# Performance work log

Measured on AMD Instinct MI355X. Metric: run time of the kernel, lower is better.

Reference implementation:

```python
import jax, jax.numpy as jnp
import numpy as np

N = 4096   # n_roi
E = 131072 # edges (avg degree 32)
B = 64     # batch of subjects/windows sharing one connectome
K = 4      # Chebyshev order


def _cheb_params(key, cin, cout):
    kw, kb = jax.random.split(key)
    w = jax.random.normal(kw, (K, cin, cout), dtype=jnp.float32) / np.sqrt(K * cin)
    b = jax.random.normal(kb, (cout,), dtype=jnp.float32) * 0.01
    return w, b


def _lin_params(key, cin, cout):
    kw, kb = jax.random.split(key)
    w = jax.random.normal(kw, (cin, cout), dtype=jnp.float32) / np.sqrt(cin)
    b = jax.random.normal(kb, (cout,), dtype=jnp.float32) * 0.01
    return w, b


def setup_inputs() -> dict:
    key = jax.random.key(0)
    ks = jax.random.split(key, 12)
    x = jax.random.normal(ks[0], (B, N, 1), dtype=jnp.float32)
    src = jax.random.randint(ks[1], (E,), 0, N, dtype=jnp.int32)
    dst = jax.random.randint(ks[2], (E,), 0, N, dtype=jnp.int32)
    edge_weight = jax.random.uniform(ks[3], (E,), dtype=jnp.float32)
    w1, b1 = _cheb_params(ks[4], 1, 32)
    w2, b2 = _cheb_params(ks[5], 32, 32)
    w3, b3 = _cheb_params(ks[6], 32, 32)
    w4, b4 = _cheb_params(ks[7], 32, 32)
    w5, b5 = _cheb_params(ks[8], 32, 4)
    fw1, fb1 = _lin_params(ks[9], N * 4, 128)
    fw2, fb2 = _lin_params(ks[10], 128, 128)
    fw3, fb3 = _lin_params(ks[11], 128, 9)
    return dict(x=x, src=src, dst=dst, edge_weight=edge_weight,
                w1=w1, b1=b1, w2=w2, b2=b2, w3=w3, b3=b3,
                w4=w4, b4=b4, w5=w5, b5=b5,
                fw1=fw1, fb1=fb1, fw2=fw2, fb2=fb2, fw3=fw3, fb3=fb3)


def _norm_weights(src, dst, edge_weight):
    # PyG ChebConv default: sym normalization, lambda_max=2 ->
    # L_hat = -D^{-1/2} A D^{-1/2}, diagonal 2/lambda_max - 1 = 0 (self-loop skipped)
    deg = jax.ops.segment_sum(edge_weight, src, num_segments=N)
    dinv = jnp.where(deg > 0, jax.lax.rsqrt(jnp.maximum(deg, 1e-30)), 0.0)
    return -dinv[src] * edge_weight * dinv[dst]


def _propagate(z, src, dst, nw):
    # z: [B, N, C] -> L_hat @ z  via gather-multiply-scatter over edges
    msg = nw[None, :, None] * z[:, src, :]          # [B, E, C]
    msg = jnp.swapaxes(msg, 0, 1)                    # [E, B, C]
    agg = jax.ops.segment_sum(msg, dst, num_segments=N)  # [N, B, C]
    return jnp.swapaxes(agg, 0, 1)                   # [B, N, C]


def _cheb_conv(x, src, dst, nw, w, b):
    # x: [B,N,Cin], w: [K,Cin,Cout]
    tx0 = x
    out = jnp.einsum('bni,io->bno', tx0, w[0])
    tx1 = _propagate(tx0, src, dst, nw)
    out = out + jnp.einsum('bni,io->bno', tx1, w[1])
    for k in range(2, K):
        tx2 = 2.0 * _propagate(tx1, src, dst, nw) - tx0
        out = out + jnp.einsum('bni,io->bno', tx2, w[k])
        tx0, tx1 = tx1, tx2
    return out + b


def reference(x, src, dst, edge_weight, w1, b1, w2, b2, w3, b3, w4, b4, w5, b5,
              fw1, fb1, fw2, fb2, fw3, fb3):
    nw = _norm_weights(src, dst, edge_weight)
    h = jax.nn.relu(_cheb_conv(x, src, dst, nw, w1, b1))
    h = jax.nn.relu(_cheb_conv(h, src, dst, nw, w2, b2))
    h = jax.nn.relu(_cheb_conv(h, src, dst, nw, w3, b3))
    h = jax.nn.relu(_cheb_conv(h, src, dst, nw, w4, b4))
    h = jax.nn.relu(_cheb_conv(h, src, dst, nw, w5, b5))  # [B, N, 4]
    h = h.reshape(B, N * 4)
    # original has dropout (identity at eval) and NO relu between fc layers
    h = h @ fw1 + fb1
    h = h @ fw2 + fb2
    return h @ fw3 + fb3  # [B, 9]
```

## Files before the change

### kernel.cpp

```cpp
#include <hip/hip_runtime.h>
#include <cstdint>

#define NN 4096
#define EE 131072
#define BB 64
#define EPAD (EE + 8 * NN)

typedef float f4 __attribute__((ext_vector_type(4)));
typedef short bf16x8 __attribute__((ext_vector_type(8)));
typedef unsigned int u4 __attribute__((ext_vector_type(4)));
typedef unsigned int u2 __attribute__((ext_vector_type(2)));
typedef unsigned short ushort_t;
typedef unsigned int uint_t;

__device__ __forceinline__ void up8(u4 u, f4& lo, f4& hi) {
    lo.x = __uint_as_float(u.x << 16);
    lo.y = __uint_as_float(u.x & 0xffff0000u);
    lo.z = __uint_as_float(u.y << 16);
    lo.w = __uint_as_float(u.y & 0xffff0000u);
    hi.x = __uint_as_float(u.z << 16);
    hi.y = __uint_as_float(u.z & 0xffff0000u);
    hi.z = __uint_as_float(u.w << 16);
    hi.w = __uint_as_float(u.w & 0xffff0000u);
}
__device__ __forceinline__ uint_t bfpk(float a, float b) {
    uint_t xa = __float_as_uint(a); xa = (xa + 0x7fffu + ((xa >> 16) & 1u)) >> 16;
    uint_t xb = __float_as_uint(b); xb = (xb + 0x7fffu + ((xb >> 16) & 1u));
    return (xa & 0xffffu) | (xb & 0xffff0000u);
}


__global__ void k_deg_hist(const int* __restrict__ src, const int* __restrict__ dst,
                           const float* __restrict__ ew, float* __restrict__ deg,
                           int* __restrict__ cnt) {
    int e = blockIdx.x * blockDim.x + threadIdx.x;
    if (e >= EE) return;
    atomicAdd(&deg[src[e]], ew[e]);
    atomicAdd(&cnt[dst[e]], 1);
}

__global__ __launch_bounds__(1024) void k_scan(const int* __restrict__ cnt,
                                               int* __restrict__ rowptr,
                                               int* __restrict__ cursor) {
    __shared__ int s[1024];
    int tid = threadIdx.x;
    int p0 = (cnt[tid * 4 + 0] + 7) & ~7;
    int p1 = (cnt[tid * 4 + 1] + 7) & ~7;
    int p2 = (cnt[tid * 4 + 2] + 7) & ~7;
    int p3 = (cnt[tid * 4 + 3] + 7) & ~7;
    int sum = p0 + p1 + p2 + p3;
    s[tid] = sum;
    __syncthreads();
    for (int off = 1; off < 1024; off <<= 1) {
        int t = (tid >= off) ? s[tid - off] : 0;
        __syncthreads();
        s[tid] += t;
        __syncthreads();
    }
    int excl = s[tid] - sum;
    rowptr[tid * 4 + 0] = excl; cursor[tid * 4 + 0] = excl; excl += p0;
    rowptr[tid * 4 + 1] = excl; cursor[tid * 4 + 1] = excl; excl += p1;
    rowptr[tid * 4 + 2] = excl; cursor[tid * 4 + 2] = excl; excl += p2;
    rowptr[tid * 4 + 3] = excl; cursor[tid * 4 + 3] = excl; excl += p3;
    if (tid == 1023) rowptr[4096] = excl;
}

__global__ void k_fill(const int* __restrict__ src, const int* __restrict__ dst,
                       const float* __restrict__ ew, const float* __restrict__ deg,
                       int* __restrict__ cursor, int2* __restrict__ cv) {
    int e = blockIdx.x * blockDim.x + threadIdx.x;
    if (e >= EE) return;
    int s = src[e], d = dst[e];
    int pos = atomicAdd(&cursor[d], 1);
    float ds = deg[s], dd = deg[d];
    float is = ds > 0.f ? rsqrtf(fmaxf(ds, 1e-30f)) : 0.f;
    float id = dd > 0.f ? rsqrtf(fmaxf(dd, 1e-30f)) : 0.f;
    float v = -(is * ew[e] * id);
    cv[pos] = make_int2(s, __float_as_int(v));
}

__global__ __launch_bounds__(256) void k_packw(const float* __restrict__ w2,
                                               const float* __restrict__ w3,
                                               const float* __restrict__ w4,
                                               const float* __restrict__ w5,
                                               uint_t* __restrict__ Wb) {
    int idx = blockIdx.x * 256 + threadIdx.x;
    int L = idx >> 11, rem = idx & 2047;
    int kk = rem >> 9, r2 = rem & 511, co = r2 >> 4, u = r2 & 15;
    float lo, hi;
    if (L < 3) {
        const float* W = (L == 0) ? w2 : (L == 1) ? w3 : w4;
        lo = W[kk * 1024 + (2 * u) * 32 + co];
        hi = W[kk * 1024 + (2 * u + 1) * 32 + co];
    } else {
        lo = (co < 4) ? w5[kk * 128 + (2 * u) * 4 + co] : 0.f;
        hi = (co < 4) ? w5[kk * 128 + (2 * u + 1) * 4 + co] : 0.f;
    }
    Wb[idx] = bfpk(lo, hi);
}

__global__ __launch_bounds__(256) void k_transpose_x(const float* __restrict__ x,
                                                     float* __restrict__ X0) {
    __shared__ float s[64 * 65];
    int n0 = blockIdx.x * 64;
    for (int idx = threadIdx.x; idx < 4096; idx += 256) {
        int b = idx >> 6, nl = idx & 63;
        s[nl * 65 + b] = x[(size_t)b * NN + n0 + nl];
    }
    __syncthreads();
    for (int idx = threadIdx.x; idx < 4096; idx += 256) {
        int nl = idx >> 6, b = idx & 63;
        X0[(size_t)(n0 + nl) * 64 + b] = s[nl * 65 + b];
    }
}

__global__ __launch_bounds__(64) void k_spmm_narrow(const int* __restrict__ rowptr,
                                                    const int2* __restrict__ cv,
                                                    const float* __restrict__ Zin,
                                                    const float* __restrict__ Tprev,
                                                    float* __restrict__ Tout,
                                                    float alpha, int useprev) {
    int n = blockIdx.x;
    int lane = threadIdx.x;
    int start = rowptr[n], end = rowptr[n + 1];
    float acc = 0.f;
    for (int e = start; e < end; e += 8) {
        const int4* q = reinterpret_cast<const int4*>(cv + e);
        int4 a = q[0], b = q[1], c = q[2], d = q[3];
        float z0 = Zin[((size_t)a.x << 6) + lane];
        float z1 = Zin[((size_t)a.z << 6) + lane];
        float z2 = Zin[((size_t)b.x << 6) + lane];
        float z3 = Zin[((size_t)b.z << 6) + lane];
        float z4 = Zin[((size_t)c.x << 6) + lane];
        float z5 = Zin[((size_t)c.z << 6) + lane];
        float z6 = Zin[((size_t)d.x << 6) + lane];
        float z7 = Zin[((size_t)d.z << 6) + lane];
        acc += __int_as_float(a.y) * z0 + __int_as_float(a.w) * z1
             + __int_as_float(b.y) * z2 + __int_as_float(b.w) * z3
             + __int_as_float(c.y) * z4 + __int_as_float(c.w) * z5
             + __int_as_float(d.y) * z6 + __int_as_float(d.w) * z7;
    }
    size_t o = ((size_t)n << 6) + lane;
    float r = alpha * acc;
    if (useprev) r -= Tprev[o];
    Tout[o] = r;
}

__global__ __launch_bounds__(256) void k_expand1(const float* __restrict__ T0,
                                                 const float* __restrict__ T1,
                                                 const float* __restrict__ T2,
                                                 const float* __restrict__ T3,
                                                 const float* __restrict__ w1,
                                                 const float* __restrict__ b1,
                                                 ushort_t* __restrict__ H) {
    __shared__ float sT[4][64];
    __shared__ float sW[128];
    __shared__ float sB[32];
    int n = blockIdx.x, tid = threadIdx.x;
    {
        int k = tid >> 6, b = tid & 63;
        const float* Tk = (k == 0) ? T0 : (k == 1) ? T1 : (k == 2) ? T2 : T3;
        sT[k][b] = Tk[(size_t)n * 64 + b];
    }
    if (tid < 128) sW[tid] = w1[tid];
    if (tid < 32) sB[tid] = b1[tid];
    __syncthreads();
    int chunk = tid >> 6, blk = tid & 63;
    int b_g = chunk * 16 + (blk & 15);
    int co0 = (blk >> 4) * 8;
    float t0 = sT[0][b_g], t1 = sT[1][b_g], t2 = sT[2][b_g], t3 = sT[3][b_g];
    float r[8];
#pragma unroll
    for (int j = 0; j < 8; ++j) {
        int co = co0 + j;
        float v = t0 * sW[co] + t1 * sW[32 + co] + t2 * sW[64 + co] + t3 * sW[96 + co] + sB[co];
        r[j] = v > 0.f ? v : 0.f;
    }
    u4 st;
    st.x = bfpk(r[0], r[1]); st.y = bfpk(r[2], r[3]);
    st.z = bfpk(r[4], r[5]); st.w = bfpk(r[6], r[7]);
    *reinterpret_cast<u4*>(H + (size_t)n * 2048 + tid * 8) = st;
}

__global__ __launch_bounds__(256, 4) void k_spmm_pure(const int* __restrict__ rowptr,
                                                      const int2* __restrict__ cv,
                                                      const ushort_t* __restrict__ Zg,
                                                      const ushort_t* __restrict__ Pown,
                                                      ushort_t* __restrict__ Tout) {
    int chunk = blockIdx.x & 3;
    int rowblk = blockIdx.x >> 2;
    int wave = threadIdx.x >> 6;
    int lane = threadIdx.x & 63;
    int n = rowblk * 4 + wave;
    int col0 = chunk * 512 + lane * 8;

    int start = rowptr[n], end = rowptr[n + 1];
    f4 aL0 = {0,0,0,0}, aH0 = {0,0,0,0}, aL1 = {0,0,0,0}, aH1 = {0,0,0,0};
    for (int e = start; e < end; e += 8) {
        const int4* q = reinterpret_cast<const int4*>(cv + e);
        int4 a = q[0], b = q[1], c = q[2], d = q[3];
        u4 u0 = *reinterpret_cast<const u4*>(Zg + (((size_t)a.x) << 11) + col0);
        u4 u1 = *reinterpret_cast<const u4*>(Zg + (((size_t)a.z) << 11) + col0);
        u4 u2 = *reinterpret_cast<const u4*>(Zg + (((size_t)b.x) << 11) + col0);
        u4 u3 = *reinterpret_cast<const u4*>(Zg + (((size_t)b.z) << 11) + col0);
        u4 u4_ = *reinterpret_cast<const u4*>(Zg + (((size_t)c.x) << 11) + col0);
        u4 u5 = *reinterpret_cast<const u4*>(Zg + (((size_t)c.z) << 11) + col0);
        u4 u6 = *reinterpret_cast<const u4*>(Zg + (((size_t)d.x) << 11) + col0);
        u4 u7 = *reinterpret_cast<const u4*>(Zg + (((size_t)d.z) << 11) + col0);
        f4 lo, hi;
        up8(u0, lo, hi);  aL0 += __int_as_float(a.y) * lo; aH0 += __int_as_float(a.y) * hi;
        up8(u1, lo, hi);  aL1 += __int_as_float(a.w) * lo; aH1 += __int_as_float(a.w) * hi;
        up8(u2, lo, hi);  aL0 += __int_as_float(b.y) * lo; aH0 += __int_as_float(b.y) * hi;
        up8(u3, lo, hi);  aL1 += __int_as_float(b.w) * lo; aH1 += __int_as_float(b.w) * hi;
        up8(u4_, lo, hi); aL0 += __int_as_float(c.y) * lo; aH0 += __int_as_float(c.y) * hi;
        up8(u5, lo, hi);  aL1 += __int_as_float(c.w) * lo; aH1 += __int_as_float(c.w) * hi;
        up8(u6, lo, hi);  aL0 += __int_as_float(d.y) * lo; aH0 += __int_as_float(d.y) * hi;
        up8(u7, lo, hi);  aL1 += __int_as_float(d.w) * lo; aH1 += __int_as_float(d.w) * hi;
    }
    size_t o = (((size_t)n) << 11) + col0;
    f4 tL = aL0 + aL1, tH = aH0 + aH1;
    if (Pown) {
        u4 pu = *reinterpret_cast<const u4*>(Pown + o);
        f4 pL, pH;
        up8(pu, pL, pH);
        tL = 2.f * tL - pL;
        tH = 2.f * tH - pH;
    }
    u4 st;
    st.x = bfpk(tL.x, tL.y); st.y = bfpk(tL.z, tL.w);
    st.z = bfpk(tH.x, tH.y); st.w = bfpk(tH.z, tH.w);
    *reinterpret_cast<u4*>(Tout + o) = st;
}

template <int COUT>
__global__ __launch_bounds__(256, 4) void k_cheb_mfma(
    const int* __restrict__ rowptr, const int2* __restrict__ cv,
    const ushort_t* __restrict__ T2g,
    const ushort_t* __restrict__ T1,
    const ushort_t* __restrict__ H,
    const uint_t* __restrict__ Wb,
    const float* __restrict__ bias,
    void* __restrict__ OUTv)
{
    int chunk = blockIdx.x & 3;
    int rowblk = blockIdx.x >> 2;
    int wave = threadIdx.x >> 6;
    int lane = threadIdx.x & 63;
    int n = rowblk * 4 + wave;
    int b16 = lane & 15, qk = lane >> 4;
    int col0 = chunk * 512 + lane * 8;
    size_t o = (((size_t)n) << 11) + col0;

    u4 a1 = *reinterpret_cast<const u4*>(T1 + o);
    u4 a2 = *reinterpret_cast<const u4*>(T2g + o);
    u4 a0 = *reinterpret_cast<const u4*>(H + o);

    int start = rowptr[n], end = rowptr[n + 1];
    f4 aL0 = {0,0,0,0}, aH0 = {0,0,0,0}, aL1 = {0,0,0,0}, aH1 = {0,0,0,0};
    for (int e = start; e < end; e += 8) {
        const int4* q = reinterpret_cast<const int4*>(cv + e);
        int4 a = q[0], b = q[1], c = q[2], d = q[3];
        u4 u0 = *reinterpret_cast<const u4*>(T2g + (((size_t)a.x) << 11) + col0);
        u4 u1 = *reinterpret_cast<const u4*>(T2g + (((size_t)a.z) << 11) + col0);
        u4 u2 = *reinterpret_cast<const u4*>(T2g + (((size_t)b.x) << 11) + col0);
        u4 u3 = *reinterpret_cast<const u4*>(T2g + (((size_t)b.z) << 11) + col0);
        u4 u4_ = *reinterpret_cast<const u4*>(T2g + (((size_t)c.x) << 11) + col0);
        u4 u5 = *reinterpret_cast<const u4*>(T2g + (((size_t)c.z) << 11) + col0);
        u4 u6 = *reinterpret_cast<const u4*>(T2g + (((size_t)d.x) << 11) + col0);
        u4 u7 = *reinterpret_cast<const u4*>(T2g + (((size_t)d.z) << 11) + col0);
        f4 lo, hi;
        up8(u0, lo, hi);  aL0 += __int_as_float(a.y) * lo; aH0 += __int_as_float(a.y) * hi;
        up8(u1, lo, hi);  aL1 += __int_as_float(a.w) * lo; aH1 += __int_as_float(a.w) * hi;
        up8(u2, lo, hi);  aL0 += __int_as_float(b.y) * lo; aH0 += __int_as_float(b.y) * hi;
        up8(u3, lo, hi);  aL1 += __int_as_float(b.w) * lo; aH1 += __int_as_float(b.w) * hi;
        up8(u4_, lo, hi); aL0 += __int_as_float(c.y) * lo; aH0 += __int_as_float(c.y) * hi;
        up8(u5, lo, hi);  aL1 += __int_as_float(c.w) * lo; aH1 += __int_as_float(c.w) * hi;
        up8(u6, lo, hi);  aL0 += __int_as_float(d.y) * lo; aH0 += __int_as_float(d.y) * hi;
        up8(u7, lo, hi);  aL1 += __int_as_float(d.w) * lo; aH1 += __int_as_float(d.w) * hi;
    }

    u4 a3;
    {
        f4 pL, pH;
        up8(a1, pL, pH);
        f4 tL = 2.f * (aL0 + aL1) - pL;
        f4 tH = 2.f * (aH0 + aH1) - pH;
        a3.x = bfpk(tL.x, tL.y); a3.y = bfpk(tL.z, tL.w);
        a3.z = bfpk(tH.x, tH.y); a3.w = bfpk(tH.z, tH.w);
    }

    const uint_t* wb = Wb + b16 * 16 + qk * 4;
    f4 accA = {0,0,0,0}, accB = {0,0,0,0};
#pragma unroll
    for (int kk = 0; kk < 4; ++kk) {
        u4 af4 = (kk == 0) ? a0 : (kk == 1) ? a1 : (kk == 2) ? a2 : a3;
        bf16x8 bf_data = *reinterpret_cast<bf16x8*>(&af4);
        u4 w0 = *reinterpret_cast<const u4*>(wb + kk * 512);
        bf16x8 af_w0 = *reinterpret_cast<bf16x8*>(&w0);
        accA = __builtin_amdgcn_mfma_f32_16x16x32_bf16(af_w0, bf_data, accA, 0, 0, 0);
        if constexpr (COUT == 32) {
            u4 w1 = *reinterpret_cast<const u4*>(wb + kk * 512 + 256);
            bf16x8 af_w1 = *reinterpret_cast<bf16x8*>(&w1);
            accB = __builtin_amdgcn_mfma_f32_16x16x32_bf16(af_w1, bf_data, accB, 0, 0, 0);
        }
    }

    if constexpr (COUT == 32) {
        f4 bA = *reinterpret_cast<const f4*>(bias + qk * 4);
        f4 bB = *reinterpret_cast<const f4*>(bias + 16 + qk * 4);
        f4 vA = accA + bA, vB = accB + bB;
        vA.x = vA.x > 0.f ? vA.x : 0.f; vA.y = vA.y > 0.f ? vA.y : 0.f;
        vA.z = vA.z > 0.f ? vA.z : 0.f; vA.w = vA.w > 0.f ? vA.w : 0.f;
        vB.x = vB.x > 0.f ? vB.x : 0.f; vB.y = vB.y > 0.f ? vB.y : 0.f;
        vB.z = vB.z > 0.f ? vB.z : 0.f; vB.w = vB.w > 0.f ? vB.w : 0.f;
        ushort_t* OB = (ushort_t*)OUTv;
        int sA = 8 * b16 + ((qk >> 1) << 7) + ((qk & 1) << 2);
        size_t obase = (((size_t)n) << 11) + chunk * 512;
        u2 pA, pB;
        pA.x = bfpk(vA.x, vA.y); pA.y = bfpk(vA.z, vA.w);
        pB.x = bfpk(vB.x, vB.y); pB.y = bfpk(vB.z, vB.w);
        *reinterpret_cast<u2*>(OB + obase + sA) = pA;
        *reinterpret_cast<u2*>(OB + obase + sA + 256) = pB;
    } else {
        if (qk == 0) {
            f4 bA = *reinterpret_cast<const f4*>(bias);
            f4 vA = accA + bA;
            vA.x = vA.x > 0.f ? vA.x : 0.f; vA.y = vA.y > 0.f ? vA.y : 0.f;
            vA.z = vA.z > 0.f ? vA.z : 0.f; vA.w = vA.w > 0.f ? vA.w : 0.f;
            float* OF = (float*)OUTv;
            *reinterpret_cast<f4*>(OF + (size_t)n * 256 + chunk * 64 + b16 * 4) = vA;
        }
    }
}

__global__ __launch_bounds__(256) void k_fc1(const float* __restrict__ H5,
                                             const float* __restrict__ fw1,
                                             float* __restrict__ fc1out) {
    __shared__ float hT[128 * 65];
    __shared__ float wS[32 * 128];
    int tid = threadIdx.x;
    int n0 = blockIdx.x * 32;
    for (int idx = tid; idx < 8192; idx += 256) {
        int n_l = idx >> 8;
        int rem = idx & 255;
        int b = rem >> 2, c = rem & 3;
        int kk = n_l * 4 + c;
        hT[kk * 65 + b] = H5[(size_t)(n0 + n_l) * 256 + rem];
    }
    float acc[8][4];
#pragma unroll
    for (int i = 0; i < 8; ++i)
#pragma unroll
        for (int j = 0; j < 4; ++j) acc[i][j] = 0.f;
    int bq = tid >> 5;
    int jq = tid & 31;
    for (int kb = 0; kb < 128; kb += 32) {
        __syncthreads();
        for (int idx = tid; idx < 4096; idx += 256) {
            int kl = idx >> 7, j = idx & 127;
            wS[idx] = fw1[(size_t)(n0 * 4 + kb + kl) * 128 + j];
        }
        __syncthreads();
        for (int kl = 0; kl < 32; ++kl) {
            int kk = kb + kl;
            float4 w = *reinterpret_cast<const float4*>(&wS[kl * 128 + jq * 4]);
#pragma unroll
            for (int bi = 0; bi < 8; ++bi) {
                float h = hT[kk * 65 + bq * 8 + bi];
                acc[bi][0] += h * w.x;
                acc[bi][1] += h * w.y;
                acc[bi][2] += h * w.z;
                acc[bi][3] += h * w.w;
            }
        }
    }
#pragma unroll
    for (int bi = 0; bi < 8; ++bi)
#pragma unroll
        for (int ji = 0; ji < 4; ++ji)
            atomicAdd(&fc1out[(bq * 8 + bi) * 128 + jq * 4 + ji], acc[bi][ji]);
}

__global__ __launch_bounds__(128) void k_fc23(const float* __restrict__ fc1out,
                                              const float* __restrict__ fb1,
                                              const float* __restrict__ fw2,
                                              const float* __restrict__ fb2,
                                              const float* __restrict__ fw3,
                                              const float* __restrict__ fb3,
                                              float* __restrict__ out) {
    int b = blockIdx.x;
    int j = threadIdx.x;
    __shared__ float r[128];
    __shared__ float s1[128];
    r[j] = fc1out[b * 128 + j] + fb1[j];
    __syncthreads();
    float acc = fb2[j];
    for (int i = 0; i < 128; ++i) acc += r[i] * fw2[i * 128 + j];
    s1[j] = acc;
    __syncthreads();
    if (j < 9) {
        float a2 = fb3[j];
        for (int i = 0; i < 128; ++i) a2 += s1[i] * fw3[i * 9 + j];
        out[b * 9 + j] = a2;
    }
}

extern "C" void kernel_launch(void* const* d_in, const int* in_sizes, int n_in,
                              void* d_out, int out_size, void* d_ws, size_t ws_size,
                              hipStream_t stream) {
    const float* x   = (const float*)d_in[0];
    const int*   src = (const int*)d_in[1];
    const int*   dst = (const int*)d_in[2];
    const float* ew  = (const float*)d_in[3];
    const float* w1  = (const float*)d_in[4];
    const float* b1  = (const float*)d_in[5];
    const float* w2  = (const float*)d_in[6];
    const float* b2  = (const float*)d_in[7];
    const float* w3  = (const float*)d_in[8];
    const float* b3  = (const float*)d_in[9];
    const float* w4  = (const float*)d_in[10];
    const float* b4  = (const float*)d_in[11];
    const float* w5  = (const float*)d_in[12];
    const float* b5  = (const float*)d_in[13];
    const float* fw1 = (const float*)d_in[14];
    const float* fb1 = (const float*)d_in[15];
    const float* fw2 = (const float*)d_in[16];
    const float* fb2 = (const float*)d_in[17];
    const float* fw3 = (const float*)d_in[18];
    const float* fb3 = (const float*)d_in[19];
    float* out = (float*)d_out;

    char* p = (char*)d_ws;
    const size_t XBYTES = (size_t)NN * 2048 * 2;
    ushort_t* X0 = (ushort_t*)(p + 0 * XBYTES);
    ushort_t* X1 = (ushort_t*)(p + 1 * XBYTES);
    ushort_t* X2 = (ushort_t*)(p + 2 * XBYTES);
    ushort_t* X3 = (ushort_t*)(p + 3 * XBYTES);
    size_t off = 4 * XBYTES;
    float* H5     = (float*)(p + off); off += (size_t)NN * 256 * 4;
    float* deg    = (float*)(p + off); off += (size_t)NN * 4;
    int*   cnt    = (int*)(p + off);   off += (size_t)NN * 4;
    int*   cursor = (int*)(p + off);   off += (size_t)NN * 4;
    int*   rowptr = (int*)(p + off);   off += (size_t)(NN + 4) * 4;
    int2*  cv     = (int2*)(p + off);  off += (size_t)EPAD * 8;
    float* fc1o   = (float*)(p + off); off += (size_t)BB * 128 * 4;
    float* xn0    = (float*)(p + off); off += (size_t)NN * 64 * 4;
    float* tn1    = (float*)(p + off); off += (size_t)NN * 64 * 4;
    float* tn2    = (float*)(p + off); off += (size_t)NN * 64 * 4;
    float* tn3    = (float*)(p + off); off += (size_t)NN * 64 * 4;
    uint_t* Wb    = (uint_t*)(p + off); off += (size_t)4 * 2048 * 4;
    if (off > ws_size) return;

    hipMemsetAsync(deg, 0, NN * 4, stream);
    hipMemsetAsync(cnt, 0, NN * 4, stream);
    hipMemsetAsync(cv, 0, (size_t)EPAD * 8, stream);
    hipMemsetAsync(fc1o, 0, BB * 128 * 4, stream);

    k_deg_hist<<<EE / 256, 256, 0, stream>>>(src, dst, ew, deg, cnt);
    k_scan<<<1, 1024, 0, stream>>>(cnt, rowptr, cursor);
    k_fill<<<EE / 256, 256, 0, stream>>>(src, dst, ew, deg, cursor, cv);
    k_packw<<<32, 256, 0, stream>>>(w2, w3, w4, w5, Wb);
    k_transpose_x<<<NN / 64, 256, 0, stream>>>(x, xn0);

    k_spmm_narrow<<<NN, 64, 0, stream>>>(rowptr, cv, xn0, nullptr, tn1, 1.f, 0);
    k_spmm_narrow<<<NN, 64, 0, stream>>>(rowptr, cv, tn1, xn0, tn2, 2.f, 1);
    k_spmm_narrow<<<NN, 64, 0, stream>>>(rowptr, cv, tn2, tn1, tn3, 2.f, 1);
    k_expand1<<<NN, 256, 0, stream>>>(xn0, tn1, tn2, tn3, w1, b1, X3);

    const int GRID4 = (NN / 4) * 4;
    auto run32 = [&](const ushort_t* H, ushort_t* T1, ushort_t* T2, ushort_t* OUT,
                     const uint_t* WbL, const float* B) {
        k_spmm_pure<<<GRID4, 256, 0, stream>>>(rowptr, cv, H, nullptr, T1);
        k_spmm_pure<<<GRID4, 256, 0, stream>>>(rowptr, cv, T1, H, T2);
        k_cheb_mfma<32><<<GRID4, 256, 0, stream>>>(rowptr, cv, T2, T1, H, WbL, B, OUT);
    };
    run32(X3, X0, X1, X2, Wb + 0 * 2048, b2);
    run32(X2, X3, X0, X1, Wb + 1 * 2048, b3);
    run32(X1, X2, X3, X0, Wb + 2 * 2048, b4);

    k_spmm_pure<<<GRID4, 256, 0, stream>>>(rowptr, cv, X0, nullptr, X1);
    k_spmm_pure<<<GRID4, 256, 0, stream>>>(rowptr, cv, X1, X0, X2);
    k_cheb_mfma<4><<<GRID4, 256, 0, stream>>>(rowptr, cv, X2, X1, X0, Wb + 3 * 2048, b5, H5);

    k_fc1<<<128, 256, 0, stream>>>(H5, fw1, fc1o);
    k_fc23<<<BB, 128, 0, stream>>>(fc1o, fb1, fw2, fb2, fw3, fb3, out);
}
```

Baseline: 571.2 us.

## Schedule SpMM rows in descending degree order via bucket-sorted permutation

Adds three small kernels that bucket nodes by padded in-degree and build a permutation with the heaviest rows first. All SpMM and Chebyshev MFMA kernels now look up their row through this permutation. The aim is better load balance, since the blocks with long edge lists get dispatched first and the tail of the grid holds only short rows. In exchange it adds a few launches, an extra indirection load per wave, and the row-to-block mapping becomes less contiguous.

```diff
diff --git a/kernel.cpp b/kernel.cpp
--- a/kernel.cpp
+++ b/kernel.cpp
@@ -79,6 +79,42 @@
     cv[pos] = make_int2(s, __float_as_int(v));
 }
 
+__global__ __launch_bounds__(256) void k_deg_buckets(const int* __restrict__ rowptr,
+                                                     int* __restrict__ bcnt) {
+    int n = blockIdx.x * 256 + threadIdx.x;
+    if (n >= NN) return;
+    int d = (rowptr[n + 1] - rowptr[n]) >> 3;
+    int b = d > 63 ? 63 : d;
+    atomicAdd(&bcnt[63 - b], 1);
+}
+
+__global__ __launch_bounds__(64) void k_scan_buckets(const int* __restrict__ bcnt,
+                                                     int* __restrict__ bcur) {
+    __shared__ int s[64];
+    int tid = threadIdx.x;
+    int v = bcnt[tid];
+    s[tid] = v;
+    __syncthreads();
+    for (int off = 1; off < 64; off <<= 1) {
+        int t = (tid >= off) ? s[tid - off] : 0;
+        __syncthreads();
+        s[tid] += t;
+        __syncthreads();
+    }
+    bcur[tid] = s[tid] - v;
+}
+
+__global__ __launch_bounds__(256) void k_scatter_perm(const int* __restrict__ rowptr,
+                                                      int* __restrict__ bcur,
+                                                      int* __restrict__ perm) {
+    int n = blockIdx.x * 256 + threadIdx.x;
+    if (n >= NN) return;
+    int d = (rowptr[n + 1] - rowptr[n]) >> 3;
+    int b = d > 63 ? 63 : d;
+    int pos = atomicAdd(&bcur[63 - b], 1);
+    perm[pos] = n;
+}
+
 __global__ __launch_bounds__(256) void k_packw(const float* __restrict__ w2,
                                                const float* __restrict__ w3,
                                                const float* __restrict__ w4,
@@ -116,11 +152,12 @@
 
 __global__ __launch_bounds__(64) void k_spmm_narrow(const int* __restrict__ rowptr,
                                                     const int2* __restrict__ cv,
+                                                    const int* __restrict__ perm,
                                                     const float* __restrict__ Zin,
                                                     const float* __restrict__ Tprev,
                                                     float* __restrict__ Tout,
                                                     float alpha, int useprev) {
-    int n = blockIdx.x;
+    int n = perm[blockIdx.x];
     int lane = threadIdx.x;
     int start = rowptr[n], end = rowptr[n + 1];
     float acc = 0.f;
@@ -184,6 +221,7 @@
 
 __global__ __launch_bounds__(256, 4) void k_spmm_pure(const int* __restrict__ rowptr,
                                                       const int2* __restrict__ cv,
+                                                      const int* __restrict__ perm,
                                                       const ushort_t* __restrict__ Zg,
                                                       const ushort_t* __restrict__ Pown,
                                                       ushort_t* __restrict__ Tout) {
@@ -191,7 +229,7 @@
     int rowblk = blockIdx.x >> 2;
     int wave = threadIdx.x >> 6;
     int lane = threadIdx.x & 63;
-    int n = rowblk * 4 + wave;
+    int n = perm[rowblk * 4 + wave];
     int col0 = chunk * 512 + lane * 8;
 
     int start = rowptr[n], end = rowptr[n + 1];
@@ -235,6 +273,7 @@
 template <int COUT>
 __global__ __launch_bounds__(256, 4) void k_cheb_mfma(
     const int* __restrict__ rowptr, const int2* __restrict__ cv,
+    const int* __restrict__ perm,
     const ushort_t* __restrict__ T2g,
     const ushort_t* __restrict__ T1,
     const ushort_t* __restrict__ H,
@@ -246,7 +285,7 @@
     int rowblk = blockIdx.x >> 2;
     int wave = threadIdx.x >> 6;
     int lane = threadIdx.x & 63;
-    int n = rowblk * 4 + wave;
+    int n = perm[rowblk * 4 + wave];
     int b16 = lane & 15, qk = lane >> 4;
     int col0 = chunk * 512 + lane * 8;
     size_t o = (((size_t)n) << 11) + col0;
@@ -449,38 +488,45 @@
     float* tn2    = (float*)(p + off); off += (size_t)NN * 64 * 4;
     float* tn3    = (float*)(p + off); off += (size_t)NN * 64 * 4;
     uint_t* Wb    = (uint_t*)(p + off); off += (size_t)4 * 2048 * 4;
+    int*   bcnt   = (int*)(p + off);   off += 64 * 4;
+    int*   bcur   = (int*)(p + off);   off += 64 * 4;
+    int*   perm   = (int*)(p + off);   off += (size_t)NN * 4;
     if (off > ws_size) return;
 
     hipMemsetAsync(deg, 0, NN * 4, stream);
     hipMemsetAsync(cnt, 0, NN * 4, stream);
     hipMemsetAsync(cv, 0, (size_t)EPAD * 8, stream);
     hipMemsetAsync(fc1o, 0, BB * 128 * 4, stream);
+    hipMemsetAsync(bcnt, 0, 64 * 4, stream);
 
     k_deg_hist<<<EE / 256, 256, 0, stream>>>(src, dst, ew, deg, cnt);
     k_scan<<<1, 1024, 0, stream>>>(cnt, rowptr, cursor);
     k_fill<<<EE / 256, 256, 0, stream>>>(src, dst, ew, deg, cursor, cv);
+    k_deg_buckets<<<NN / 256, 256, 0, stream>>>(rowptr, bcnt);
+    k_scan_buckets<<<1, 64, 0, stream>>>(bcnt, bcur);
+    k_scatter_perm<<<NN / 256, 256, 0, stream>>>(rowptr, bcur, perm);
     k_packw<<<32, 256, 0, stream>>>(w2, w3, w4, w5, Wb);
     k_transpose_x<<<NN / 64, 256, 0, stream>>>(x, xn0);
 
-    k_spmm_narrow<<<NN, 64, 0, stream>>>(rowptr, cv, xn0, nullptr, tn1, 1.f, 0);
-    k_spmm_narrow<<<NN, 64, 0, stream>>>(rowptr, cv, tn1, xn0, tn2, 2.f, 1);
-    k_spmm_narrow<<<NN, 64, 0, stream>>>(rowptr, cv, tn2, tn1, tn3, 2.f, 1);
+    k_spmm_narrow<<<NN, 64, 0, stream>>>(rowptr, cv, perm, xn0, nullptr, tn1, 1.f, 0);
+    k_spmm_narrow<<<NN, 64, 0, stream>>>(rowptr, cv, perm, tn1, xn0, tn2, 2.f, 1);
+    k_spmm_narrow<<<NN, 64, 0, stream>>>(rowptr, cv, perm, tn2, tn1, tn3, 2.f, 1);
     k_expand1<<<NN, 256, 0, stream>>>(xn0, tn1, tn2, tn3, w1, b1, X3);
 
     const int GRID4 = (NN / 4) * 4;
     auto run32 = [&](const ushort_t* H, ushort_t* T1, ushort_t* T2, ushort_t* OUT,
                      const uint_t* WbL, const float* B) {
-        k_spmm_pure<<<GRID4, 256, 0, stream>>>(rowptr, cv, H, nullptr, T1);
-        k_spmm_pure<<<GRID4, 256, 0, stream>>>(rowptr, cv, T1, H, T2);
-        k_cheb_mfma<32><<<GRID4, 256, 0, stream>>>(rowptr, cv, T2, T1, H, WbL, B, OUT);
+        k_spmm_pure<<<GRID4, 256, 0, stream>>>(rowptr, cv, perm, H, nullptr, T1);
+        k_spmm_pure<<<GRID4, 256, 0, stream>>>(rowptr, cv, perm, T1, H, T2);
+        k_cheb_mfma<32><<<GRID4, 256, 0, stream>>>(rowptr, cv, perm, T2, T1, H, WbL, B, OUT);
     };
     run32(X3, X0, X1, X2, Wb + 0 * 2048, b2);
     run32(X2, X3, X0, X1, Wb + 1 * 2048, b3);
     run32(X1, X2, X3, X0, Wb + 2 * 2048, b4);
 
-    k_spmm_pure<<<GRID4, 256, 0, stream>>>(rowptr, cv, X0, nullptr, X1);
-    k_spmm_pure<<<GRID4, 256, 0, stream>>>(rowptr, cv, X1, X0, X2);
-    k_cheb_mfma<4><<<GRID4, 256, 0, stream>>>(rowptr, cv, X2, X1, X0, Wb + 3 * 2048, b5, H5);
+    k_spmm_pure<<<GRID4, 256, 0, stream>>>(rowptr, cv, perm, X0, nullptr, X1);
+    k_spmm_pure<<<GRID4, 256, 0, stream>>>(rowptr, cv, perm, X1, X0, X2);
+    k_cheb_mfma<4><<<GRID4, 256, 0, stream>>>(rowptr, cv, perm, X2, X1, X0, Wb + 3 * 2048, b5, H5);
 
     k_fc1<<<128, 256, 0, stream>>>(H5, fw1, fc1o);
     k_fc23<<<BB, 128, 0, stream>>>(fc1o, fb1, fw2, fb2, fw3, fb3, out);
```

Measured after the change: 621.8 us. 1.09x slower.
